# Kernel tuning notes

Hardware: AMD Instinct MI355X
Metric: run time of the kernel (lower is better)

Reference implementation:

```python
import jax, jax.numpy as jnp
import numpy as np

N, C, P, M = 8, 20, 8732, 16
THRESHOLD, NEG_POS_RATIO, ALPHA = 0.5, 3, 1.0


def cxcy_to_xy(c):
    return jnp.concatenate([c[..., :2] - c[..., 2:] / 2.0, c[..., :2] + c[..., 2:] / 2.0], axis=-1)


def xy_to_cxcy(xy):
    return jnp.concatenate([(xy[..., :2] + xy[..., 2:]) / 2.0, xy[..., 2:] - xy[..., :2]], axis=-1)


def cxcy_to_gcxgcy(cxcy, priors):
    g_cxcy = (cxcy[..., :2] - priors[..., :2]) / (priors[..., 2:] / 10.0)
    g_wh = jnp.log(cxcy[..., 2:] / priors[..., 2:]) * 5.0
    return jnp.concatenate([g_cxcy, g_wh], axis=-1)


def jaccard(a, b):
    # a: (M,4), b: (P,4), boundary coords -> IoU (M,P)
    lo = jnp.maximum(a[:, None, :2], b[None, :, :2])
    hi = jnp.minimum(a[:, None, 2:], b[None, :, 2:])
    inter = jnp.prod(jnp.clip(hi - lo, 0.0), axis=-1)
    area_a = jnp.prod(a[:, 2:] - a[:, :2], axis=-1)
    area_b = jnp.prod(b[:, 2:] - b[:, :2], axis=-1)
    return inter / (area_a[:, None] + area_b[None, :] - inter)


def setup_inputs() -> dict:
    key = jax.random.key(0)
    k1, k2, k3, k4, k5, k6 = jax.random.split(key, 6)
    predicted_locs = jax.random.normal(k1, (N, C, P, 4), jnp.float32)
    predicted_scores = jax.random.normal(k2, (N, C, P, 2), jnp.float32)
    # valid ground-truth boundary boxes (x1<x2, y1<y2) in [0,1]
    ctr = jax.random.uniform(k3, (N, C, M, 2), minval=0.2, maxval=0.8)
    wh = jax.random.uniform(k4, (N, C, M, 2), minval=0.05, maxval=0.3)
    boxes = jnp.concatenate([ctr - wh / 2.0, ctr + wh / 2.0], axis=-1)
    # valid priors in cxcywh (w,h > 0 so log-encoding is finite)
    pctr = jax.random.uniform(k5, (P, 2), minval=0.05, maxval=0.95)
    pwh = jax.random.uniform(k6, (P, 2), minval=0.05, maxval=0.5)
    priors_cxcy = jnp.concatenate([pctr, pwh], axis=-1)
    labels = jnp.ones((N, C, M), jnp.int32)  # binary per-class head: object label = 1
    return {
        "predicted_locs": predicted_locs,
        "predicted_scores": predicted_scores,
        "boxes": boxes,
        "labels": labels,
        "priors_cxcy": priors_cxcy,
    }


def _forward(predicted_locs, predicted_scores, boxes, priors_cxcy, labels):
    n_classes = predicted_scores.shape[1]
    n_priors = predicted_scores.shape[2]
    priors_xy = cxcy_to_xy(priors_cxcy)

    def match(b, lab):
        # b: (M,4) boundary, lab: (M,) int
        ov = jaccard(b, priors_xy)                       # (M,P)
        obj_for_prior = jnp.argmax(ov, axis=0)           # (P,)
        ov_for_prior = jnp.max(ov, axis=0)               # (P,)
        prior_for_obj = jnp.argmax(ov, axis=1)           # (M,)
        # force each object to own its best prior
        obj_for_prior = obj_for_prior.at[prior_for_obj].set(jnp.arange(b.shape[0]))
        ov_for_prior = ov_for_prior.at[prior_for_obj].set(1.0)
        cls = jnp.where(ov_for_prior < THRESHOLD, 0, lab[obj_for_prior])  # (P,)
        tl = cxcy_to_gcxgcy(xy_to_cxcy(b[obj_for_prior]), priors_cxcy)    # (P,4)
        return tl, cls

    true_locs, true_classes = jax.vmap(jax.vmap(match))(boxes, labels)  # (N,C,P,4), (N,C,P)

    pos = true_classes != 0                      # (N,C,P)
    posf = pos.astype(predicted_locs.dtype)
    n_pos_bc = posf.sum(axis=2)                  # (N,C) positives per image per class
    n_pos_c = n_pos_bc.sum(axis=0)               # (C,)

    # localization: mean L1 over positive priors (4 coords each), per class
    l1 = jnp.abs(predicted_locs - true_locs).sum(-1) * posf   # (N,C,P)
    loc_loss_c = l1.sum(axis=(0, 2)) / jnp.maximum(n_pos_c * 4.0, 1.0)

    # per-prior binary cross entropy
    logp = jax.nn.log_softmax(predicted_scores, axis=-1)      # (N,C,P,2)
    ce = -jnp.take_along_axis(logp, true_classes[..., None], axis=-1)[..., 0]  # (N,C,P)
    conf_pos_c = (ce * posf).sum(axis=(0, 2))

    # hard negative mining: sort negatives desc per (image,class) row, keep top 3*n_pos
    ce_neg = jnp.where(pos, 0.0, ce)
    ce_neg_sorted = -jnp.sort(-ce_neg, axis=-1)               # (N,C,P) descending
    n_hard = NEG_POS_RATIO * n_pos_bc                         # (N,C)
    ranks = jnp.arange(n_priors, dtype=n_hard.dtype)
    hard_mask = ranks[None, None, :] < n_hard[..., None]
    conf_hard_c = (ce_neg_sorted * hard_mask).sum(axis=(0, 2))

    safe = jnp.maximum(n_pos_c, 1.0)
    loss_c = jnp.where(
        n_pos_c > 0,
        (conf_pos_c + conf_hard_c + ALPHA * loc_loss_c) / safe,
        0.0,
    ) / n_classes
    return loss_c.sum()


def reference(predicted_locs, predicted_scores, boxes, labels, priors_cxcy):
    return _forward(predicted_locs, predicted_scores, boxes, priors_cxcy, labels)
```

## Files before the change

kernel.cpp:

```cpp
#include <hip/hip_runtime.h>
#include <math.h>

#define NN 8
#define CC 20
#define PP 8732
#define MM 16
#define NPR 3
#define SPLIT 8
#define CH 1092
#define HALFB 0x3f000000u
#define ROWS (NN * CC)

__device__ __forceinline__ float lse2(float a, float b) {
    float mx = fmaxf(a, b);
    return mx + logf(expf(a - mx) + expf(b - mx));
}

#define ABLK 256
__global__ __launch_bounds__(ABLK) void mbox_p1(
    const float* __restrict__ locs, const float* __restrict__ scores,
    const float* __restrict__ boxes, const int* __restrict__ labels,
    const float* __restrict__ priors,
    unsigned int* __restrict__ packed, unsigned long long* __restrict__ partials,
    float* __restrict__ cstats)
{
    const int row = blockIdx.x / SPLIT;
    const int chunk = blockIdx.x - row * SPLIT;
    const int tid = threadIdx.x, lane = tid & 63, wav = tid >> 6;
    __shared__ float s_bx1[MM], s_by1[MM], s_bx2[MM], s_by2[MM], s_area[MM];
    __shared__ float s_bcx[MM], s_bcy[MM], s_bw[MM], s_bh[MM];
    __shared__ int s_lab[MM];
    __shared__ unsigned long long s_pk[4 * MM];
    __shared__ float s_rf[4 * 3];

    if (tid < MM) {
        const float* b = boxes + ((size_t)row * MM + tid) * 4;
        float x1 = b[0], y1 = b[1], x2 = b[2], y2 = b[3];
        s_bx1[tid] = x1; s_by1[tid] = y1; s_bx2[tid] = x2; s_by2[tid] = y2;
        s_area[tid] = (x2 - x1) * (y2 - y1);
        s_bcx[tid] = (x1 + x2) * 0.5f; s_bcy[tid] = (y1 + y2) * 0.5f;
        s_bw[tid] = x2 - x1; s_bh[tid] = y2 - y1;
        s_lab[tid] = labels[row * MM + tid];
    }
    __syncthreads();

    const float4* pri4 = (const float4*)priors;
    const float4* loc4 = (const float4*)(locs + (size_t)row * PP * 4);
    const float2* sc2  = (const float2*)(scores + (size_t)row * PP * 2);
    unsigned int* pk   = packed + (size_t)row * PP;

    float bestv[MM]; int bestp[MM];
#pragma unroll
    for (int m = 0; m < MM; m++) { bestv[m] = -1.0f; bestp[m] = 0x7fffffff; }
    float l_np = 0.0f, l_l1 = 0.0f, l_cp = 0.0f;
    const int p0 = chunk * CH, p1 = min(p0 + CH, PP);

    for (int p = p0 + tid; p < p1; p += ABLK) {
        float4 pr = pri4[p];
        float px1 = pr.x - pr.z * 0.5f, py1 = pr.y - pr.w * 0.5f;
        float px2 = pr.x + pr.z * 0.5f, py2 = pr.y + pr.w * 0.5f;
        float area_b = (px2 - px1) * (py2 - py1);
        float bov = -1.0f; int bm = 0;
#pragma unroll
        for (int m = 0; m < MM; m++) {
            float dx = fminf(s_bx2[m], px2) - fmaxf(s_bx1[m], px1);
            float dy = fminf(s_by2[m], py2) - fmaxf(s_by1[m], py1);
            dx = fmaxf(dx, 0.0f); dy = fmaxf(dy, 0.0f);
            float inter = dx * dy;
            float iou = inter / (s_area[m] + area_b - inter);
            if (iou > bov) { bov = iou; bm = m; }
            if (iou > bestv[m]) { bestv[m] = iou; bestp[m] = p; }
        }
        pk[p] = (__float_as_uint(bov) & ~31u) | (unsigned)bm;
        if (bov >= 0.5f && s_lab[bm] != 0) {
            float2 sc = sc2[p];
            l_cp += lse2(sc.x, sc.y) - sc.y;
            l_np += 1.0f;
            float4 pl = loc4[p];
            float tx = (s_bcx[bm] - pr.x) * 10.0f / pr.z;
            float ty = (s_bcy[bm] - pr.y) * 10.0f / pr.w;
            float tw = logf(s_bw[bm] / pr.z) * 5.0f;
            float th = logf(s_bh[bm] / pr.w) * 5.0f;
            l_l1 += fabsf(pl.x - tx) + fabsf(pl.y - ty) + fabsf(pl.z - tw) + fabsf(pl.w - th);
        }
    }

#pragma unroll
    for (int m = 0; m < MM; m++) {
        unsigned long long key =
            ((unsigned long long)__float_as_uint(bestv[m]) << 32) |
            (unsigned)(0x7fffffff - bestp[m]);
#pragma unroll
        for (int off = 32; off; off >>= 1) {
            unsigned long long o = __shfl_down(key, off);
            if (o > key) key = o;
        }
        if (lane == 0) s_pk[wav * MM + m] = key;
    }
#pragma unroll
    for (int off = 32; off; off >>= 1) {
        l_np += __shfl_down(l_np, off);
        l_l1 += __shfl_down(l_l1, off);
        l_cp += __shfl_down(l_cp, off);
    }
    if (lane == 0) { s_rf[wav * 3] = l_np; s_rf[wav * 3 + 1] = l_l1; s_rf[wav * 3 + 2] = l_cp; }
    __syncthreads();
    if (tid < MM) {
        unsigned long long key = s_pk[tid];
        for (int w = 1; w < 4; w++) {
            unsigned long long o = s_pk[w * MM + tid];
            if (o > key) key = o;
        }
        partials[((size_t)row * MM + tid) * SPLIT + chunk] = key;
    }
    if (tid == 0) {
        float np = 0, l1 = 0, cp = 0;
        for (int w = 0; w < 4; w++) { np += s_rf[w * 3]; l1 += s_rf[w * 3 + 1]; cp += s_rf[w * 3 + 2]; }
        float* cs = cstats + ((size_t)row * SPLIT + chunk) * 3;
        cs[0] = np; cs[1] = l1; cs[2] = cp;
    }
}

__global__ __launch_bounds__(64) void mbox_force(
    const float* __restrict__ locs, const float* __restrict__ scores,
    const float* __restrict__ boxes, const int* __restrict__ labels,
    const float* __restrict__ priors, unsigned int* __restrict__ packed,
    const unsigned long long* __restrict__ partials,
    const float* __restrict__ cstats, float* __restrict__ rstats)
{
    const int row = blockIdx.x, tid = threadIdx.x;
    __shared__ float s_bcx[MM], s_bcy[MM], s_bw[MM], s_bh[MM];
    __shared__ int s_lab[MM], s_pfo[MM];
    __shared__ float s_sum[3];
    if (tid < MM) {
        const float* b = boxes + ((size_t)row * MM + tid) * 4;
        float x1 = b[0], y1 = b[1], x2 = b[2], y2 = b[3];
        s_bcx[tid] = (x1 + x2) * 0.5f; s_bcy[tid] = (y1 + y2) * 0.5f;
        s_bw[tid] = x2 - x1; s_bh[tid] = y2 - y1;
        s_lab[tid] = labels[row * MM + tid];
        unsigned long long key = partials[((size_t)row * MM + tid) * SPLIT];
        for (int c2 = 1; c2 < SPLIT; c2++) {
            unsigned long long o = partials[((size_t)row * MM + tid) * SPLIT + c2];
            if (o > key) key = o;
        }
        s_pfo[tid] = 0x7fffffff - (int)(unsigned)(key & 0xffffffffull);
    }
    if (tid >= 16 && tid < 19) {
        int j = tid - 16; float s = 0;
        for (int c2 = 0; c2 < SPLIT; c2++) s += cstats[((size_t)row * SPLIT + c2) * 3 + j];
        s_sum[j] = s;
    }
    __syncthreads();

    const float4* pri4 = (const float4*)priors;
    const float4* loc4 = (const float4*)(locs + (size_t)row * PP * 4);
    const float2* sc2  = (const float2*)(scores + (size_t)row * PP * 2);
    unsigned int* pk   = packed + (size_t)row * PP;

    float d_np = 0, d_l1 = 0, d_cp = 0;
    int p = -1; bool is_last = false;
    if (tid < MM) {
        p = s_pfo[tid];
        is_last = true;
        for (int mm = tid + 1; mm < MM; mm++) if (s_pfo[mm] == p) is_last = false;
        if (is_last) {
            unsigned int u = pk[p];
            float4 pr = pri4[p];
            float4 pl = loc4[p];
            float2 sc = sc2[p];
            float lse = lse2(sc.x, sc.y);
            int mo = u & 31;
            bool po = ((u & ~31u) >= HALFB) && (s_lab[mo] != 0);
            if (po) {
                d_np -= 1.0f; d_cp -= (lse - sc.y);
                float tx = (s_bcx[mo] - pr.x) * 10.0f / pr.z;
                float ty = (s_bcy[mo] - pr.y) * 10.0f / pr.w;
                float tw = logf(s_bw[mo] / pr.z) * 5.0f;
                float th = logf(s_bh[mo] / pr.w) * 5.0f;
                d_l1 -= fabsf(pl.x - tx) + fabsf(pl.y - ty) + fabsf(pl.z - tw) + fabsf(pl.w - th);
            }
            if (s_lab[tid] != 0) {
                d_np += 1.0f; d_cp += (lse - sc.y);
                float tx = (s_bcx[tid] - pr.x) * 10.0f / pr.z;
                float ty = (s_bcy[tid] - pr.y) * 10.0f / pr.w;
                float tw = logf(s_bw[tid] / pr.z) * 5.0f;
                float th = logf(s_bh[tid] / pr.w) * 5.0f;
                d_l1 += fabsf(pl.x - tx) + fabsf(pl.y - ty) + fabsf(pl.z - tw) + fabsf(pl.w - th);
            }
        }
    }
    __syncthreads();
    if (tid < MM && is_last) pk[p] = 0x3f800000u | (unsigned)tid;

#pragma unroll
    for (int off = 32; off; off >>= 1) {
        d_np += __shfl_down(d_np, off);
        d_l1 += __shfl_down(d_l1, off);
        d_cp += __shfl_down(d_cp, off);
    }
    if (tid == 0) {
        float* rs = rstats + (size_t)row * 8;
        rs[0] = s_sum[0] + d_np;
        rs[1] = s_sum[1] + d_l1;
        rs[2] = s_sum[2] + d_cp;
    }
}

#define CBLK 1024
#define CNW 16
__global__ __launch_bounds__(CBLK) void mbox_sel(
    const float* __restrict__ scores, const int* __restrict__ labels,
    const unsigned int* __restrict__ packed, float* __restrict__ rstats)
{
    const int row = blockIdx.x, tid = threadIdx.x, lane = tid & 63, wav = tid >> 6;
    __shared__ float s_ce[PP];
    __shared__ int s_lab[MM];
    __shared__ unsigned int s_hist[256];
    __shared__ unsigned int s_prefix, s_Kr;
    __shared__ int s_Ksh;
    __shared__ float s_rf[CNW];
    __shared__ int s_ri[CNW];

    if (tid < MM) s_lab[tid] = labels[row * MM + tid];
    if (tid == 0) {
        float np = rstats[(size_t)row * 8];
        int K = NPR * (int)(np + 0.5f);
        s_Ksh = K; s_prefix = 0u; s_Kr = (unsigned)(K > 0 ? K : 0);
    }
    __syncthreads();

    const float2* sc2 = (const float2*)(scores + (size_t)row * PP * 2);
    const unsigned int* pk = packed + (size_t)row * PP;
    for (int p = tid; p < PP; p += CBLK) {
        unsigned int u = pk[p];
        float2 sc = sc2[p];
        int m = u & 31;
        bool pos = ((u & ~31u) >= HALFB) && (s_lab[m] != 0);
        s_ce[p] = pos ? 0.0f : fmaxf(lse2(sc.x, sc.y) - sc.x, 0.0f);
    }
    __syncthreads();
    const int K = s_Ksh;

    unsigned int pivot = 0u;
    if (K > 0 && K < PP) {
        for (int pass = 0; pass < 4; pass++) {
            const int shift = 24 - 8 * pass;
            if (tid < 256) s_hist[tid] = 0u;
            __syncthreads();
            const unsigned int pref   = s_prefix;
            const unsigned int maskhi = (pass == 0) ? 0u : (0xffffffffu << (shift + 8));
            for (int p = tid; p < PP; p += CBLK) {
                unsigned int u = __float_as_uint(s_ce[p]);
                if ((u & maskhi) == pref) atomicAdd(&s_hist[(u >> shift) & 255u], 1u);
            }
            __syncthreads();
            if (wav == 0) {
                unsigned int Kr = s_Kr;
                unsigned int h0 = s_hist[lane * 4 + 0];
                unsigned int h1 = s_hist[lane * 4 + 1];
                unsigned int h2 = s_hist[lane * 4 + 2];
                unsigned int h3 = s_hist[lane * 4 + 3];
                unsigned int c3 = h3;
                unsigned int c2 = h3 + h2;
                unsigned int c1 = c2 + h1;
                unsigned int c0 = c1 + h0;
                unsigned int suf = c0;
#pragma unroll
                for (int off = 1; off < 64; off <<= 1) {
                    unsigned int o = __shfl_down(suf, off);
                    if (lane + off < 64) suf += o;
                }
                unsigned int above = suf - c0;
                int cand = -1;
                unsigned int G = 0;
                if      (c3 + above >= Kr) { cand = lane * 4 + 3; G = above + c3 - h3; }
                else if (c2 + above >= Kr) { cand = lane * 4 + 2; G = above + c2 - h2; }
                else if (c1 + above >= Kr) { cand = lane * 4 + 1; G = above + c1 - h1; }
                else if (c0 + above >= Kr) { cand = lane * 4 + 0; G = above + c0 - h0; }
                int best = cand;
#pragma unroll
                for (int off = 32; off; off >>= 1) best = max(best, __shfl_down(best, off));
                best = __shfl(best, 0);
                if (cand == best && cand >= 0) {
                    s_Kr = Kr - G;
                    s_prefix = pref | ((unsigned int)best << shift);
                }
            }
            __syncthreads();
        }
        pivot = s_prefix;
    }

    float sgt = 0.0f; int cgt = 0;
    for (int p = tid; p < PP; p += CBLK) {
        float v = s_ce[p];
        if (__float_as_uint(v) > pivot) { sgt += v; cgt++; }
    }
#pragma unroll
    for (int off = 32; off; off >>= 1) {
        sgt += __shfl_down(sgt, off);
        cgt += __shfl_down(cgt, off);
    }
    if (lane == 0) { s_rf[wav] = sgt; s_ri[wav] = cgt; }
    __syncthreads();
    if (tid == 0) {
        float s = 0; int cnt = 0;
        for (int w = 0; w < CNW; w++) { s += s_rf[w]; cnt += s_ri[w]; }
        float chard = (K <= 0) ? 0.0f : (s + (float)(K - cnt) * __uint_as_float(pivot));
        rstats[(size_t)row * 8 + 4] = chard;
    }
}

__global__ void mbox_finalize(const float* __restrict__ rstats, float* __restrict__ out) {
    int c = threadIdx.x;
    float loss = 0.0f;
    if (c < CC) {
        float np = 0, l1 = 0, cp = 0, ch = 0;
        for (int n = 0; n < NN; n++) {
            const float* s = rstats + ((size_t)(n * CC + c)) * 8;
            np += s[0]; l1 += s[1]; cp += s[2]; ch += s[4];
        }
        float loc = l1 / fmaxf(np * 4.0f, 1.0f);
        float val = (np > 0.0f) ? (cp + ch + loc) / fmaxf(np, 1.0f) : 0.0f;
        loss = val / (float)CC;
    }
#pragma unroll
    for (int off = 32; off; off >>= 1) loss += __shfl_down(loss, off);
    if (threadIdx.x == 0) out[0] = loss;
}

extern "C" void kernel_launch(void* const* d_in, const int* in_sizes, int n_in,
                              void* d_out, int out_size, void* d_ws, size_t ws_size,
                              hipStream_t stream) {
    const float* locs   = (const float*)d_in[0];
    const float* scores = (const float*)d_in[1];
    const float* boxes  = (const float*)d_in[2];
    const int*   labels = (const int*)d_in[3];
    const float* priors = (const float*)d_in[4];
    float* out = (float*)d_out;

    char* ws = (char*)d_ws;
    unsigned int* packed        = (unsigned int*)ws;
    unsigned long long* partials= (unsigned long long*)(ws + 5588480);
    float* cstats               = (float*)(ws + 5588480 + 163840);
    float* rstats               = (float*)(ws + 5588480 + 163840 + 15360);

    mbox_p1<<<ROWS * SPLIT, ABLK, 0, stream>>>(locs, scores, boxes, labels, priors,
                                               packed, partials, cstats);
    mbox_force<<<ROWS, 64, 0, stream>>>(locs, scores, boxes, labels, priors,
                                        packed, partials, cstats, rstats);
    mbox_sel<<<ROWS, CBLK, 0, stream>>>(scores, labels, packed, rstats);
    mbox_finalize<<<1, 64, 0, stream>>>(rstats, out);
}
```

Before: 142.1 us.

## Fuse force-match into selection kernel and use register-resident radix-4 threshold search

```diff
diff --git a/kernel.cpp b/kernel.cpp
--- a/kernel.cpp
+++ b/kernel.cpp
@@ -8,12 +8,14 @@
 #define NPR 3
 #define SPLIT 8
 #define CH 1092
-#define HALFB 0x3f000000u
 #define ROWS (NN * CC)
+
+__device__ __forceinline__ float fast_rcp(float x) { return __builtin_amdgcn_rcpf(x); }
 
 __device__ __forceinline__ float lse2(float a, float b) {
     float mx = fmaxf(a, b);
-    return mx + logf(expf(a - mx) + expf(b - mx));
+    float d  = fabsf(a - b);
+    return mx + logf(1.0f + expf(-d));
 }
 
 #define ABLK 256
@@ -21,11 +23,11 @@
     const float* __restrict__ locs, const float* __restrict__ scores,
     const float* __restrict__ boxes, const int* __restrict__ labels,
     const float* __restrict__ priors,
-    unsigned int* __restrict__ packed, unsigned long long* __restrict__ partials,
-    float* __restrict__ cstats)
+    unsigned char* __restrict__ pk8, float* __restrict__ ce0,
+    unsigned long long* __restrict__ partials, float* __restrict__ cstats)
 {
-    const int row = blockIdx.x / SPLIT;
-    const int chunk = blockIdx.x - row * SPLIT;
+    const int row = blockIdx.x >> 3;
+    const int chunk = blockIdx.x & 7;
     const int tid = threadIdx.x, lane = tid & 63, wav = tid >> 6;
     __shared__ float s_bx1[MM], s_by1[MM], s_bx2[MM], s_by2[MM], s_area[MM];
     __shared__ float s_bcx[MM], s_bcy[MM], s_bw[MM], s_bh[MM];
@@ -47,18 +49,20 @@
     const float4* pri4 = (const float4*)priors;
     const float4* loc4 = (const float4*)(locs + (size_t)row * PP * 4);
     const float2* sc2  = (const float2*)(scores + (size_t)row * PP * 2);
-    unsigned int* pk   = packed + (size_t)row * PP;
+    unsigned char* pk  = pk8 + (size_t)row * PP;
+    float* cer         = ce0 + (size_t)row * PP;
 
     float bestv[MM]; int bestp[MM];
 #pragma unroll
     for (int m = 0; m < MM; m++) { bestv[m] = -1.0f; bestp[m] = 0x7fffffff; }
     float l_np = 0.0f, l_l1 = 0.0f, l_cp = 0.0f;
-    const int p0 = chunk * CH, p1 = min(p0 + CH, PP);
-
-    for (int p = p0 + tid; p < p1; p += ABLK) {
+    const int p0 = chunk * CH, p1e = min(p0 + CH, PP);
+
+    for (int p = p0 + tid; p < p1e; p += ABLK) {
         float4 pr = pri4[p];
-        float px1 = pr.x - pr.z * 0.5f, py1 = pr.y - pr.w * 0.5f;
-        float px2 = pr.x + pr.z * 0.5f, py2 = pr.y + pr.w * 0.5f;
+        float hw = pr.z * 0.5f, hh = pr.w * 0.5f;
+        float px1 = pr.x - hw, py1 = pr.y - hh;
+        float px2 = pr.x + hw, py2 = pr.y + hh;
         float area_b = (px2 - px1) * (py2 - py1);
         float bov = -1.0f; int bm = 0;
 #pragma unroll
@@ -67,15 +71,19 @@
             float dy = fminf(s_by2[m], py2) - fmaxf(s_by1[m], py1);
             dx = fmaxf(dx, 0.0f); dy = fmaxf(dy, 0.0f);
             float inter = dx * dy;
-            float iou = inter / (s_area[m] + area_b - inter);
+            float den = s_area[m] + area_b - inter;
+            float iou = inter * fast_rcp(den);
             if (iou > bov) { bov = iou; bm = m; }
             if (iou > bestv[m]) { bestv[m] = iou; bestp[m] = p; }
         }
-        pk[p] = (__float_as_uint(bov) & ~31u) | (unsigned)bm;
-        if (bov >= 0.5f && s_lab[bm] != 0) {
-            float2 sc = sc2[p];
-            l_cp += lse2(sc.x, sc.y) - sc.y;
+        float2 sc = sc2[p];
+        float lse = lse2(sc.x, sc.y);
+        bool pos = (bov >= 0.5f) && (s_lab[bm] != 0);
+        pk[p]  = (unsigned char)((pos ? 16u : 0u) | (unsigned)bm);
+        cer[p] = pos ? 0.0f : fmaxf(lse - sc.x, 0.0f);
+        if (pos) {
             l_np += 1.0f;
+            l_cp += lse - sc.y;
             float4 pl = loc4[p];
             float tx = (s_bcx[bm] - pr.x) * 10.0f / pr.z;
             float ty = (s_bcy[bm] - pr.y) * 10.0f / pr.w;
@@ -121,57 +129,58 @@
     }
 }
 
-__global__ __launch_bounds__(64) void mbox_force(
+#define CBLK 1024
+#define EPT 9
+__global__ __launch_bounds__(CBLK) void mbox_sel(
     const float* __restrict__ locs, const float* __restrict__ scores,
     const float* __restrict__ boxes, const int* __restrict__ labels,
-    const float* __restrict__ priors, unsigned int* __restrict__ packed,
+    const float* __restrict__ priors,
+    const unsigned char* __restrict__ pk8, const float* __restrict__ ce0,
     const unsigned long long* __restrict__ partials,
     const float* __restrict__ cstats, float* __restrict__ rstats)
 {
-    const int row = blockIdx.x, tid = threadIdx.x;
+    const int row = blockIdx.x, tid = threadIdx.x, lane = tid & 63, wav = tid >> 6;
     __shared__ float s_bcx[MM], s_bcy[MM], s_bw[MM], s_bh[MM];
-    __shared__ int s_lab[MM], s_pfo[MM];
-    __shared__ float s_sum[3];
+    __shared__ int s_lab[MM], s_pfo[MM], s_fp[MM];
+    __shared__ float s_fv[MM], s_sum[3];
+    __shared__ unsigned int s_cnt[16][4];
+    __shared__ unsigned int s_K;
+    __shared__ float s_redf[16];
+    __shared__ int s_redi[16];
+
+    if (tid < 64) ((unsigned int*)s_cnt)[tid] = 0u;
     if (tid < MM) {
+        s_fp[tid] = -1;
         const float* b = boxes + ((size_t)row * MM + tid) * 4;
         float x1 = b[0], y1 = b[1], x2 = b[2], y2 = b[3];
         s_bcx[tid] = (x1 + x2) * 0.5f; s_bcy[tid] = (y1 + y2) * 0.5f;
         s_bw[tid] = x2 - x1; s_bh[tid] = y2 - y1;
         s_lab[tid] = labels[row * MM + tid];
-        unsigned long long key = partials[((size_t)row * MM + tid) * SPLIT];
-        for (int c2 = 1; c2 < SPLIT; c2++) {
-            unsigned long long o = partials[((size_t)row * MM + tid) * SPLIT + c2];
-            if (o > key) key = o;
-        }
+        const unsigned long long* pr = partials + ((size_t)row * MM + tid) * SPLIT;
+        unsigned long long key = pr[0];
+        for (int c = 1; c < SPLIT; c++) { unsigned long long o = pr[c]; if (o > key) key = o; }
         s_pfo[tid] = 0x7fffffff - (int)(unsigned)(key & 0xffffffffull);
     }
     if (tid >= 16 && tid < 19) {
         int j = tid - 16; float s = 0;
-        for (int c2 = 0; c2 < SPLIT; c2++) s += cstats[((size_t)row * SPLIT + c2) * 3 + j];
+        for (int c = 0; c < SPLIT; c++) s += cstats[((size_t)row * SPLIT + c) * 3 + j];
         s_sum[j] = s;
     }
     __syncthreads();
 
-    const float4* pri4 = (const float4*)priors;
-    const float4* loc4 = (const float4*)(locs + (size_t)row * PP * 4);
-    const float2* sc2  = (const float2*)(scores + (size_t)row * PP * 2);
-    unsigned int* pk   = packed + (size_t)row * PP;
-
     float d_np = 0, d_l1 = 0, d_cp = 0;
-    int p = -1; bool is_last = false;
     if (tid < MM) {
-        p = s_pfo[tid];
-        is_last = true;
+        int p = s_pfo[tid];
+        bool is_last = true;
         for (int mm = tid + 1; mm < MM; mm++) if (s_pfo[mm] == p) is_last = false;
         if (is_last) {
-            unsigned int u = pk[p];
-            float4 pr = pri4[p];
-            float4 pl = loc4[p];
-            float2 sc = sc2[p];
+            const float4 pr = ((const float4*)priors)[p];
+            const float4 pl = ((const float4*)(locs + (size_t)row * PP * 4))[p];
+            const float2 sc = ((const float2*)(scores + (size_t)row * PP * 2))[p];
             float lse = lse2(sc.x, sc.y);
-            int mo = u & 31;
-            bool po = ((u & ~31u) >= HALFB) && (s_lab[mo] != 0);
-            if (po) {
+            unsigned int u = pk8[(size_t)row * PP + p];
+            if (u & 16u) {
+                int mo = u & 15;
                 d_np -= 1.0f; d_cp -= (lse - sc.y);
                 float tx = (s_bcx[mo] - pr.x) * 10.0f / pr.z;
                 float ty = (s_bcy[mo] - pr.y) * 10.0f / pr.w;
@@ -186,127 +195,97 @@
                 float tw = logf(s_bw[tid] / pr.z) * 5.0f;
                 float th = logf(s_bh[tid] / pr.w) * 5.0f;
                 d_l1 += fabsf(pl.x - tx) + fabsf(pl.y - ty) + fabsf(pl.z - tw) + fabsf(pl.w - th);
-            }
-        }
-    }
-    __syncthreads();
-    if (tid < MM && is_last) pk[p] = 0x3f800000u | (unsigned)tid;
-
-#pragma unroll
-    for (int off = 32; off; off >>= 1) {
-        d_np += __shfl_down(d_np, off);
-        d_l1 += __shfl_down(d_l1, off);
-        d_cp += __shfl_down(d_cp, off);
-    }
-    if (tid == 0) {
-        float* rs = rstats + (size_t)row * 8;
-        rs[0] = s_sum[0] + d_np;
-        rs[1] = s_sum[1] + d_l1;
-        rs[2] = s_sum[2] + d_cp;
-    }
-}
-
-#define CBLK 1024
-#define CNW 16
-__global__ __launch_bounds__(CBLK) void mbox_sel(
-    const float* __restrict__ scores, const int* __restrict__ labels,
-    const unsigned int* __restrict__ packed, float* __restrict__ rstats)
-{
-    const int row = blockIdx.x, tid = threadIdx.x, lane = tid & 63, wav = tid >> 6;
-    __shared__ float s_ce[PP];
-    __shared__ int s_lab[MM];
-    __shared__ unsigned int s_hist[256];
-    __shared__ unsigned int s_prefix, s_Kr;
-    __shared__ int s_Ksh;
-    __shared__ float s_rf[CNW];
-    __shared__ int s_ri[CNW];
-
-    if (tid < MM) s_lab[tid] = labels[row * MM + tid];
-    if (tid == 0) {
-        float np = rstats[(size_t)row * 8];
-        int K = NPR * (int)(np + 0.5f);
-        s_Ksh = K; s_prefix = 0u; s_Kr = (unsigned)(K > 0 ? K : 0);
-    }
-    __syncthreads();
-
-    const float2* sc2 = (const float2*)(scores + (size_t)row * PP * 2);
-    const unsigned int* pk = packed + (size_t)row * PP;
-    for (int p = tid; p < PP; p += CBLK) {
-        unsigned int u = pk[p];
-        float2 sc = sc2[p];
-        int m = u & 31;
-        bool pos = ((u & ~31u) >= HALFB) && (s_lab[m] != 0);
-        s_ce[p] = pos ? 0.0f : fmaxf(lse2(sc.x, sc.y) - sc.x, 0.0f);
-    }
-    __syncthreads();
-    const int K = s_Ksh;
-
-    unsigned int pivot = 0u;
-    if (K > 0 && K < PP) {
-        for (int pass = 0; pass < 4; pass++) {
-            const int shift = 24 - 8 * pass;
-            if (tid < 256) s_hist[tid] = 0u;
+                s_fv[tid] = 0.0f;
+            } else {
+                s_fv[tid] = fmaxf(lse - sc.x, 0.0f);
+            }
+            s_fp[tid] = p;
+        }
+    }
+    if (tid < 64) {
+#pragma unroll
+        for (int off = 32; off; off >>= 1) {
+            d_np += __shfl_down(d_np, off);
+            d_l1 += __shfl_down(d_l1, off);
+            d_cp += __shfl_down(d_cp, off);
+        }
+        if (tid == 0) {
+            float np = s_sum[0] + d_np;
+            rstats[(size_t)row * 8 + 0] = np;
+            rstats[(size_t)row * 8 + 1] = s_sum[1] + d_l1;
+            rstats[(size_t)row * 8 + 2] = s_sum[2] + d_cp;
+            int K = NPR * (int)(np + 0.5f);
+            s_K = (K > 0) ? (unsigned)K : 0u;
+        }
+    }
+    __syncthreads();
+
+    const float* cer = ce0 + (size_t)row * PP;
+    unsigned int uv[EPT];
+#pragma unroll
+    for (int k = 0; k < EPT; k++) {
+        int p = tid + k * CBLK;
+        uv[k] = (p < PP) ? __float_as_uint(cer[p]) : 0u;
+    }
+    for (int t = 0; t < MM; t++) {
+        int fp = s_fp[t];
+        if (fp >= 0) {
+            unsigned int fb = __float_as_uint(s_fv[t]);
+#pragma unroll
+            for (int k = 0; k < EPT; k++) if (tid + k * CBLK == fp) uv[k] = fb;
+        }
+    }
+
+    const unsigned int K = s_K;
+    unsigned int T = 0u;
+    if (K > 0u) {
+        for (int r = 0; r < 16; r++) {
+            const int b = 30 - 2 * r;
+            const unsigned int T1 = T | (1u << b), T2 = T | (2u << b), T3 = T | (3u << b);
+            unsigned int c1 = 0, c2 = 0, c3 = 0;
+#pragma unroll
+            for (int k = 0; k < EPT; k++) {
+                unsigned int u = uv[k];
+                c1 += (u >= T1); c2 += (u >= T2); c3 += (u >= T3);
+            }
+#pragma unroll
+            for (int off = 32; off; off >>= 1) {
+                c1 += __shfl_down(c1, off);
+                c2 += __shfl_down(c2, off);
+                c3 += __shfl_down(c3, off);
+            }
+            if (lane == 0) {
+                atomicAdd(&s_cnt[r][1], c1);
+                atomicAdd(&s_cnt[r][2], c2);
+                atomicAdd(&s_cnt[r][3], c3);
+            }
             __syncthreads();
-            const unsigned int pref   = s_prefix;
-            const unsigned int maskhi = (pass == 0) ? 0u : (0xffffffffu << (shift + 8));
-            for (int p = tid; p < PP; p += CBLK) {
-                unsigned int u = __float_as_uint(s_ce[p]);
-                if ((u & maskhi) == pref) atomicAdd(&s_hist[(u >> shift) & 255u], 1u);
-            }
-            __syncthreads();
-            if (wav == 0) {
-                unsigned int Kr = s_Kr;
-                unsigned int h0 = s_hist[lane * 4 + 0];
-                unsigned int h1 = s_hist[lane * 4 + 1];
-                unsigned int h2 = s_hist[lane * 4 + 2];
-                unsigned int h3 = s_hist[lane * 4 + 3];
-                unsigned int c3 = h3;
-                unsigned int c2 = h3 + h2;
-                unsigned int c1 = c2 + h1;
-                unsigned int c0 = c1 + h0;
-                unsigned int suf = c0;
-#pragma unroll
-                for (int off = 1; off < 64; off <<= 1) {
-                    unsigned int o = __shfl_down(suf, off);
-                    if (lane + off < 64) suf += o;
-                }
-                unsigned int above = suf - c0;
-                int cand = -1;
-                unsigned int G = 0;
-                if      (c3 + above >= Kr) { cand = lane * 4 + 3; G = above + c3 - h3; }
-                else if (c2 + above >= Kr) { cand = lane * 4 + 2; G = above + c2 - h2; }
-                else if (c1 + above >= Kr) { cand = lane * 4 + 1; G = above + c1 - h1; }
-                else if (c0 + above >= Kr) { cand = lane * 4 + 0; G = above + c0 - h0; }
-                int best = cand;
-#pragma unroll
-                for (int off = 32; off; off >>= 1) best = max(best, __shfl_down(best, off));
-                best = __shfl(best, 0);
-                if (cand == best && cand >= 0) {
-                    s_Kr = Kr - G;
-                    s_prefix = pref | ((unsigned int)best << shift);
-                }
-            }
-            __syncthreads();
-        }
-        pivot = s_prefix;
+            unsigned int C1 = s_cnt[r][1], C2 = s_cnt[r][2], C3 = s_cnt[r][3];
+            if      (C3 >= K) T = T3;
+            else if (C2 >= K) T = T2;
+            else if (C1 >= K) T = T1;
+        }
     }
 
     float sgt = 0.0f; int cgt = 0;
-    for (int p = tid; p < PP; p += CBLK) {
-        float v = s_ce[p];
-        if (__float_as_uint(v) > pivot) { sgt += v; cgt++; }
+    if (K > 0u) {
+#pragma unroll
+        for (int k = 0; k < EPT; k++) {
+            unsigned int u = uv[k];
+            if (u > T) { sgt += __uint_as_float(u); cgt++; }
+        }
     }
 #pragma unroll
     for (int off = 32; off; off >>= 1) {
         sgt += __shfl_down(sgt, off);
         cgt += __shfl_down(cgt, off);
     }
-    if (lane == 0) { s_rf[wav] = sgt; s_ri[wav] = cgt; }
+    if (lane == 0) { s_redf[wav] = sgt; s_redi[wav] = cgt; }
     __syncthreads();
     if (tid == 0) {
         float s = 0; int cnt = 0;
-        for (int w = 0; w < CNW; w++) { s += s_rf[w]; cnt += s_ri[w]; }
-        float chard = (K <= 0) ? 0.0f : (s + (float)(K - cnt) * __uint_as_float(pivot));
+        for (int w = 0; w < 16; w++) { s += s_redf[w]; cnt += s_redi[w]; }
+        float chard = (K > 0u) ? (s + (float)(int)(K - (unsigned)cnt) * __uint_as_float(T)) : 0.0f;
         rstats[(size_t)row * 8 + 4] = chard;
     }
 }
@@ -340,15 +319,15 @@
     float* out = (float*)d_out;
 
     char* ws = (char*)d_ws;
-    unsigned int* packed        = (unsigned int*)ws;
-    unsigned long long* partials= (unsigned long long*)(ws + 5588480);
-    float* cstats               = (float*)(ws + 5588480 + 163840);
-    float* rstats               = (float*)(ws + 5588480 + 163840 + 15360);
+    float* ce0                   = (float*)ws;
+    unsigned char* pk8           = (unsigned char*)(ws + 5588480);
+    unsigned long long* partials = (unsigned long long*)(ws + 6985600);
+    float* cstats                = (float*)(ws + 7149440);
+    float* rstats                = (float*)(ws + 7164800);
 
     mbox_p1<<<ROWS * SPLIT, ABLK, 0, stream>>>(locs, scores, boxes, labels, priors,
-                                               packed, partials, cstats);
-    mbox_force<<<ROWS, 64, 0, stream>>>(locs, scores, boxes, labels, priors,
-                                        packed, partials, cstats, rstats);
-    mbox_sel<<<ROWS, CBLK, 0, stream>>>(scores, labels, packed, rstats);
+                                               pk8, ce0, partials, cstats);
+    mbox_sel<<<ROWS, CBLK, 0, stream>>>(locs, scores, boxes, labels, priors,
+                                        pk8, ce0, partials, cstats, rstats);
     mbox_finalize<<<1, 64, 0, stream>>>(rstats, out);
 }
```

New measurement: 149.9 us. 5.5% more time.
